# Kernel tuning notes

Measured on AMD Instinct MI355X. Metric: run time of the kernel, lower is better.

The kernel has to match this reference:

```python
import jax, jax.numpy as jnp
import numpy as np

N_NODES = 100000
N_EDGES = 625000
EMB_DIM = 128
ALPHA = 0.8  # alpha in original; effective scale is alpha/2 = 0.4


def setup_inputs() -> dict:
    key = jax.random.key(0)
    k1, k2, k3, k4, k5 = jax.random.split(key, 5)
    x = jax.random.normal(k1, (N_NODES, EMB_DIM), dtype=jnp.float32)
    e = jax.random.normal(k2, (N_NODES, EMB_DIM), dtype=jnp.float32)
    hg_vals = jax.random.uniform(k3, (N_EDGES,), dtype=jnp.float32)
    hg_rows = jax.random.randint(k4, (N_EDGES,), 0, N_NODES, dtype=jnp.int32)
    hg_cols = jax.random.randint(k5, (N_EDGES,), 0, N_NODES, dtype=jnp.int32)
    t = jnp.zeros((), dtype=jnp.float32)
    return {"t": t, "x": x, "e": e, "hg_vals": hg_vals,
            "hg_rows": hg_rows, "hg_cols": hg_cols}


def reference(t, x, e, hg_vals, hg_rows, hg_cols):
    # f = spmm((alpha/2) * HG, x) - x + e, with alpha = 0.8 (constant per entry)
    n = x.shape[0]
    scale = ALPHA / 2.0
    # gather source node features per nonzero, scale by edge value
    msgs = (scale * hg_vals)[:, None] * x[hg_cols]          # [nnz, d]
    prop = jax.ops.segment_sum(msgs, hg_rows, num_segments=n)  # [N, d]
    return prop - x + e
```

## Files before the change

### kernel.cpp

```cpp
#include <hip/hip_runtime.h>
#include <hip/hip_fp16.h>


#define EMB_DIM 128
#define Q_SLOTS 32
#define CAP 16
#define OVF_MAX 8192

struct __align__(8) half4_t { __half2 a, b; };
typedef float f32x4 __attribute__((ext_vector_type(4)));

__global__ void prep_kernel(const int* __restrict__ rows,
                            const int* __restrict__ cols,
                            const float* __restrict__ vals,
                            int* __restrict__ counts,
                            int2* __restrict__ slots,
                            int* __restrict__ ovf_cursor,
                            int4* __restrict__ ovf,
                            int n_edges,
                            const f32x4* __restrict__ x4,
                            half4_t* __restrict__ xh4,
                            int n_x4) {
    int i = blockIdx.x * blockDim.x + threadIdx.x;
    if (i < n_x4) {
        f32x4 f = __builtin_nontemporal_load(x4 + i);
        half4_t h;
        h.a = __floats2half2_rn(f.x, f.y);
        h.b = __floats2half2_rn(f.z, f.w);
        xh4[i] = h;
    }
    if (i < n_edges) {
        int   r  = __builtin_nontemporal_load(rows + i);
        int   c  = __builtin_nontemporal_load(cols + i);
        float vv = __builtin_nontemporal_load(vals + i);
        int2 p;
        p.x = c;
        p.y = __float_as_int(0.4f * vv);
        int pos = atomicAdd(&counts[r], 1);
        if (pos < CAP) {
            slots[(size_t)r * CAP + pos] = p;
        } else {
            int o = atomicAdd(ovf_cursor, 1);
            if (o < OVF_MAX) ovf[o] = make_int4(r, p.x, p.y, 0);
        }
    }
}

__global__ void gather_fp16_kernel(const half4_t* __restrict__ xh4,
                                   const f32x4* __restrict__ e4,
                                   const int* __restrict__ counts,
                                   const int2* __restrict__ slots,
                                   const int* __restrict__ ovf_cursor,
                                   const int4* __restrict__ ovf,
                                   f32x4* __restrict__ out4, int n_nodes) {
    int tid = blockIdx.x * blockDim.x + threadIdx.x;
    int row = tid >> 5;
    int q   = tid & 31;
    if (row >= n_nodes) return;

    int cfull = counts[row];
    int n = (cfull < CAP) ? cfull : CAP;
    const long long* b = (const long long*)(slots + (size_t)row * CAP);

    long long pp = 0;
    if (q < n) pp = __builtin_nontemporal_load(b + q);
    int myc = (int)(pp & 0xffffffffLL);
    int myv = (int)(pp >> 32);

    float4 acc = make_float4(0.f, 0.f, 0.f, 0.f);
    int nm1 = n - 1;

    for (int base = 0; base < n; base += 8) {
        int   col[8];
        float v[8];
#pragma unroll
        for (int k = 0; k < 8; ++k) {
            int j  = base + k;
            int jc = (j < n) ? j : nm1;
            col[k] = __shfl(myc, jc, 32);
            int vi = __shfl(myv, jc, 32);
            v[k]   = (j < n) ? __int_as_float(vi) : 0.f;
        }
        half4_t hv[8];
#pragma unroll
        for (int k = 0; k < 8; ++k) {
            hv[k] = xh4[col[k] * Q_SLOTS + q];
        }
#pragma unroll
        for (int k = 0; k < 8; ++k) {
            float2 f0 = __half22float2(hv[k].a);
            float2 f1 = __half22float2(hv[k].b);
            acc.x = fmaf(v[k], f0.x, acc.x);
            acc.y = fmaf(v[k], f0.y, acc.y);
            acc.z = fmaf(v[k], f1.x, acc.z);
            acc.w = fmaf(v[k], f1.y, acc.w);
        }
    }

    if (cfull > CAP) {
        int cnt = *ovf_cursor;
        cnt = (cnt < OVF_MAX) ? cnt : OVF_MAX;
        for (int k = 0; k < cnt; ++k) {
            int4 en = ovf[k];
            if (en.x == row) {
                float vv = __int_as_float(en.z);
                half4_t hv = xh4[en.y * Q_SLOTS + q];
                float2 f0 = __half22float2(hv.a);
                float2 f1 = __half22float2(hv.b);
                acc.x = fmaf(vv, f0.x, acc.x);
                acc.y = fmaf(vv, f0.y, acc.y);
                acc.z = fmaf(vv, f1.x, acc.z);
                acc.w = fmaf(vv, f1.y, acc.w);
            }
        }
    }

    int idx = row * Q_SLOTS + q;
    half4_t hx = xh4[idx];
    float2 x0 = __half22float2(hx.a);
    float2 x1 = __half22float2(hx.b);
    f32x4 er = __builtin_nontemporal_load(e4 + idx);
    f32x4 o;
    o.x = acc.x + er.x - x0.x;
    o.y = acc.y + er.y - x0.y;
    o.z = acc.z + er.z - x1.x;
    o.w = acc.w + er.w - x1.y;
    __builtin_nontemporal_store(o, out4 + idx);
}

__global__ void gather_f32_kernel(const f32x4* __restrict__ x4,
                                  const f32x4* __restrict__ e4,
                                  const int* __restrict__ counts,
                                  const int2* __restrict__ slots,
                                  const int* __restrict__ ovf_cursor,
                                  const int4* __restrict__ ovf,
                                  f32x4* __restrict__ out4, int n_nodes) {
    int tid = blockIdx.x * blockDim.x + threadIdx.x;
    int row = tid >> 5;
    int q   = tid & 31;
    if (row >= n_nodes) return;

    int cfull = counts[row];
    int n = (cfull < CAP) ? cfull : CAP;
    const long long* b = (const long long*)(slots + (size_t)row * CAP);

    long long pp = 0;
    if (q < n) pp = __builtin_nontemporal_load(b + q);
    int myc = (int)(pp & 0xffffffffLL);
    int myv = (int)(pp >> 32);

    float4 acc = make_float4(0.f, 0.f, 0.f, 0.f);
    int nm1 = n - 1;

    for (int base = 0; base < n; base += 8) {
        int   col[8];
        float v[8];
#pragma unroll
        for (int k = 0; k < 8; ++k) {
            int j  = base + k;
            int jc = (j < n) ? j : nm1;
            col[k] = __shfl(myc, jc, 32);
            int vi = __shfl(myv, jc, 32);
            v[k]   = (j < n) ? __int_as_float(vi) : 0.f;
        }
        f32x4 xv[8];
#pragma unroll
        for (int k = 0; k < 8; ++k) {
            xv[k] = x4[col[k] * Q_SLOTS + q];
        }
#pragma unroll
        for (int k = 0; k < 8; ++k) {
            acc.x = fmaf(v[k], xv[k].x, acc.x);
            acc.y = fmaf(v[k], xv[k].y, acc.y);
            acc.z = fmaf(v[k], xv[k].z, acc.z);
            acc.w = fmaf(v[k], xv[k].w, acc.w);
        }
    }

    if (cfull > CAP) {
        int cnt = *ovf_cursor;
        cnt = (cnt < OVF_MAX) ? cnt : OVF_MAX;
        for (int k = 0; k < cnt; ++k) {
            int4 en = ovf[k];
            if (en.x == row) {
                float vv = __int_as_float(en.z);
                f32x4 m = x4[en.y * Q_SLOTS + q];
                acc.x = fmaf(vv, m.x, acc.x);
                acc.y = fmaf(vv, m.y, acc.y);
                acc.z = fmaf(vv, m.z, acc.z);
                acc.w = fmaf(vv, m.w, acc.w);
            }
        }
    }

    int idx = row * Q_SLOTS + q;
    f32x4 xr = x4[idx];
    f32x4 er = __builtin_nontemporal_load(e4 + idx);
    f32x4 o;
    o.x = acc.x + er.x - xr.x;
    o.y = acc.y + er.y - xr.y;
    o.z = acc.z + er.z - xr.z;
    o.w = acc.w + er.w - xr.w;
    __builtin_nontemporal_store(o, out4 + idx);
}

__global__ void build_chain_kernel(const int* __restrict__ rows,
                                   const int* __restrict__ cols,
                                   const float* __restrict__ vals,
                                   int* __restrict__ head,
                                   int4* __restrict__ nodes, int n_edges) {
    int i = blockIdx.x * blockDim.x + threadIdx.x;
    if (i >= n_edges) return;
    int r = rows[i];
    int prev = atomicExch(&head[r], i);
    nodes[i] = make_int4(cols[i], __float_as_int(0.4f * vals[i]), prev, 0);
}
__global__ void gather_chain_kernel(const float2* __restrict__ x2,
                                    const float2* __restrict__ e2,
                                    const int* __restrict__ head,
                                    const int4* __restrict__ nodes,
                                    float2* __restrict__ out2, int n_nodes) {
    int tid = blockIdx.x * blockDim.x + threadIdx.x;
    int row = tid >> 6, q = tid & 63;
    if (row >= n_nodes) return;
    float2 acc = make_float2(0.f, 0.f);
    int j = head[row];
    if (j >= 0) {
        int4 nd = nodes[j];
        for (;;) {
            int4 nd2;
            bool more = (nd.z >= 0);
            if (more) nd2 = nodes[nd.z];
            float v = __int_as_float(nd.y);
            float2 xv = x2[nd.x * 64 + q];
            acc.x = fmaf(v, xv.x, acc.x);
            acc.y = fmaf(v, xv.y, acc.y);
            if (!more) break;
            nd = nd2;
        }
    }
    int idx = row * 64 + q;
    float2 xr = x2[idx], er = e2[idx];
    out2[idx] = make_float2(acc.x + er.x - xr.x, acc.y + er.y - xr.y);
}

extern "C" void kernel_launch(void* const* d_in, const int* in_sizes, int n_in,
                              void* d_out, int out_size, void* d_ws, size_t ws_size,
                              hipStream_t stream) {
    const float* x    = (const float*)d_in[1];
    const float* e    = (const float*)d_in[2];
    const float* vals = (const float*)d_in[3];
    const int*   rows = (const int*)d_in[4];
    const int*   cols = (const int*)d_in[5];
    float* out = (float*)d_out;

    const int n_edges = in_sizes[3];
    const int n_nodes = in_sizes[1] / EMB_DIM;
    const int n_x4    = n_nodes * Q_SLOTS;

    size_t need_a = (size_t)OVF_MAX * sizeof(int4) +
                    (size_t)n_x4 * sizeof(half4_t) +
                    (size_t)n_nodes * CAP * sizeof(int2) +
                    (size_t)(n_nodes + 1) * sizeof(int);
    size_t need_b = (size_t)OVF_MAX * sizeof(int4) +
                    (size_t)n_nodes * CAP * sizeof(int2) +
                    (size_t)(n_nodes + 1) * sizeof(int);

    if (ws_size >= need_a) {
        int4*    ovf        = (int4*)d_ws;
        half4_t* xh4        = (half4_t*)(ovf + OVF_MAX);
        int2*    slots      = (int2*)(xh4 + (size_t)n_x4);
        int*     counts     = (int*)(slots + (size_t)n_nodes * CAP);
        int*     ovf_cursor = counts + n_nodes;

        hipMemsetAsync(counts, 0, (size_t)(n_nodes + 1) * sizeof(int), stream);

        int pt = (n_x4 > n_edges) ? n_x4 : n_edges;
        int pb = (pt + 255) / 256;
        prep_kernel<<<pb, 256, 0, stream>>>(rows, cols, vals, counts, slots,
                                            ovf_cursor, ovf, n_edges,
                                            (const f32x4*)x, xh4, n_x4);

        long long gt = (long long)n_nodes * 32;
        int gb = (int)((gt + 255) / 256);
        gather_fp16_kernel<<<gb, 256, 0, stream>>>(xh4, (const f32x4*)e,
                                                   counts, slots,
                                                   ovf_cursor, ovf,
                                                   (f32x4*)out, n_nodes);
    } else if (ws_size >= need_b) {
        int4* ovf        = (int4*)d_ws;
        int2* slots      = (int2*)(ovf + OVF_MAX);
        int*  counts     = (int*)(slots + (size_t)n_nodes * CAP);
        int*  ovf_cursor = counts + n_nodes;

        hipMemsetAsync(counts, 0, (size_t)(n_nodes + 1) * sizeof(int), stream);

        int eb = (n_edges + 255) / 256;
        prep_kernel<<<eb, 256, 0, stream>>>(rows, cols, vals, counts, slots,
                                            ovf_cursor, ovf, n_edges,
                                            (const f32x4*)x, (half4_t*)0, 0);

        long long gt = (long long)n_nodes * 32;
        int gb = (int)((gt + 255) / 256);
        gather_f32_kernel<<<gb, 256, 0, stream>>>((const f32x4*)x,
                                                  (const f32x4*)e,
                                                  counts, slots,
                                                  ovf_cursor, ovf,
                                                  (f32x4*)out, n_nodes);
    } else {
        int4* nodes = (int4*)d_ws;
        int*  head  = (int*)(nodes + n_edges);
        hipMemsetAsync(head, 0xFF, (size_t)n_nodes * sizeof(int), stream);
        int eb = (n_edges + 255) / 256;
        build_chain_kernel<<<eb, 256, 0, stream>>>(rows, cols, vals, head,
                                                   nodes, n_edges);
        long long gt = (long long)n_nodes * 64;
        int gb = (int)((gt + 255) / 256);
        gather_chain_kernel<<<gb, 256, 0, stream>>>((const float2*)x,
                                                    (const float2*)e,
                                                    head, nodes,
                                                    (float2*)out, n_nodes);
    }
}
```

Before: 209.1 us.

## Bin edges into 32-row coarse buckets and sort within block in LDS

Result: slower. 238.5 us (+14.1%).

```diff
diff --git a/kernel.cpp b/kernel.cpp
--- a/kernel.cpp
+++ b/kernel.cpp
@@ -4,17 +4,19 @@
 
 #define EMB_DIM 128
 #define Q_SLOTS 32
-#define CAP 16
+#define RPB 32
+#define CAP_C 384
 #define OVF_MAX 8192
 
 struct __align__(8) half4_t { __half2 a, b; };
 typedef float f32x4 __attribute__((ext_vector_type(4)));
+typedef unsigned long long u64;
 
 __global__ void prep_kernel(const int* __restrict__ rows,
                             const int* __restrict__ cols,
                             const float* __restrict__ vals,
-                            int* __restrict__ counts,
-                            int2* __restrict__ slots,
+                            int* __restrict__ ccnt,
+                            u64* __restrict__ coarse,
                             int* __restrict__ ovf_cursor,
                             int4* __restrict__ ovf,
                             int n_edges,
@@ -33,175 +35,141 @@
         int   r  = __builtin_nontemporal_load(rows + i);
         int   c  = __builtin_nontemporal_load(cols + i);
         float vv = __builtin_nontemporal_load(vals + i);
-        int2 p;
-        p.x = c;
-        p.y = __float_as_int(0.4f * vv);
-        int pos = atomicAdd(&counts[r], 1);
-        if (pos < CAP) {
-            slots[(size_t)r * CAP + pos] = p;
+        int b = r >> 5;
+        int pos = atomicAdd(&ccnt[b], 1);
+        unsigned lo = (unsigned)(c | ((r & (RPB - 1)) << 17));
+        unsigned hi = (unsigned)__float_as_int(0.4f * vv);
+        u64 pv = (u64)lo | ((u64)hi << 32);
+        if (pos < CAP_C) {
+            __builtin_nontemporal_store(pv, coarse + (size_t)b * CAP_C + pos);
         } else {
             int o = atomicAdd(ovf_cursor, 1);
-            if (o < OVF_MAX) ovf[o] = make_int4(r, p.x, p.y, 0);
-        }
-    }
-}
-
-__global__ void gather_fp16_kernel(const half4_t* __restrict__ xh4,
-                                   const f32x4* __restrict__ e4,
-                                   const int* __restrict__ counts,
-                                   const int2* __restrict__ slots,
-                                   const int* __restrict__ ovf_cursor,
-                                   const int4* __restrict__ ovf,
-                                   f32x4* __restrict__ out4, int n_nodes) {
-    int tid = blockIdx.x * blockDim.x + threadIdx.x;
-    int row = tid >> 5;
-    int q   = tid & 31;
-    if (row >= n_nodes) return;
-
-    int cfull = counts[row];
-    int n = (cfull < CAP) ? cfull : CAP;
-    const long long* b = (const long long*)(slots + (size_t)row * CAP);
-
-    long long pp = 0;
-    if (q < n) pp = __builtin_nontemporal_load(b + q);
-    int myc = (int)(pp & 0xffffffffLL);
-    int myv = (int)(pp >> 32);
-
-    float4 acc = make_float4(0.f, 0.f, 0.f, 0.f);
-    int nm1 = n - 1;
-
-    for (int base = 0; base < n; base += 8) {
-        int   col[8];
-        float v[8];
-#pragma unroll
-        for (int k = 0; k < 8; ++k) {
-            int j  = base + k;
-            int jc = (j < n) ? j : nm1;
-            col[k] = __shfl(myc, jc, 32);
-            int vi = __shfl(myv, jc, 32);
-            v[k]   = (j < n) ? __int_as_float(vi) : 0.f;
-        }
-        half4_t hv[8];
-#pragma unroll
-        for (int k = 0; k < 8; ++k) {
-            hv[k] = xh4[col[k] * Q_SLOTS + q];
-        }
-#pragma unroll
-        for (int k = 0; k < 8; ++k) {
-            float2 f0 = __half22float2(hv[k].a);
-            float2 f1 = __half22float2(hv[k].b);
-            acc.x = fmaf(v[k], f0.x, acc.x);
-            acc.y = fmaf(v[k], f0.y, acc.y);
-            acc.z = fmaf(v[k], f1.x, acc.z);
-            acc.w = fmaf(v[k], f1.y, acc.w);
-        }
-    }
-
-    if (cfull > CAP) {
-        int cnt = *ovf_cursor;
-        cnt = (cnt < OVF_MAX) ? cnt : OVF_MAX;
-        for (int k = 0; k < cnt; ++k) {
-            int4 en = ovf[k];
-            if (en.x == row) {
-                float vv = __int_as_float(en.z);
-                half4_t hv = xh4[en.y * Q_SLOTS + q];
-                float2 f0 = __half22float2(hv.a);
-                float2 f1 = __half22float2(hv.b);
-                acc.x = fmaf(vv, f0.x, acc.x);
-                acc.y = fmaf(vv, f0.y, acc.y);
-                acc.z = fmaf(vv, f1.x, acc.z);
-                acc.w = fmaf(vv, f1.y, acc.w);
-            }
-        }
-    }
-
-    int idx = row * Q_SLOTS + q;
-    half4_t hx = xh4[idx];
-    float2 x0 = __half22float2(hx.a);
-    float2 x1 = __half22float2(hx.b);
-    f32x4 er = __builtin_nontemporal_load(e4 + idx);
-    f32x4 o;
-    o.x = acc.x + er.x - x0.x;
-    o.y = acc.y + er.y - x0.y;
-    o.z = acc.z + er.z - x1.x;
-    o.w = acc.w + er.w - x1.y;
-    __builtin_nontemporal_store(o, out4 + idx);
-}
-
-__global__ void gather_f32_kernel(const f32x4* __restrict__ x4,
-                                  const f32x4* __restrict__ e4,
-                                  const int* __restrict__ counts,
-                                  const int2* __restrict__ slots,
-                                  const int* __restrict__ ovf_cursor,
-                                  const int4* __restrict__ ovf,
-                                  f32x4* __restrict__ out4, int n_nodes) {
-    int tid = blockIdx.x * blockDim.x + threadIdx.x;
-    int row = tid >> 5;
-    int q   = tid & 31;
-    if (row >= n_nodes) return;
-
-    int cfull = counts[row];
-    int n = (cfull < CAP) ? cfull : CAP;
-    const long long* b = (const long long*)(slots + (size_t)row * CAP);
-
-    long long pp = 0;
-    if (q < n) pp = __builtin_nontemporal_load(b + q);
-    int myc = (int)(pp & 0xffffffffLL);
-    int myv = (int)(pp >> 32);
-
-    float4 acc = make_float4(0.f, 0.f, 0.f, 0.f);
-    int nm1 = n - 1;
-
-    for (int base = 0; base < n; base += 8) {
-        int   col[8];
-        float v[8];
-#pragma unroll
-        for (int k = 0; k < 8; ++k) {
-            int j  = base + k;
-            int jc = (j < n) ? j : nm1;
-            col[k] = __shfl(myc, jc, 32);
-            int vi = __shfl(myv, jc, 32);
-            v[k]   = (j < n) ? __int_as_float(vi) : 0.f;
-        }
-        f32x4 xv[8];
-#pragma unroll
-        for (int k = 0; k < 8; ++k) {
-            xv[k] = x4[col[k] * Q_SLOTS + q];
-        }
-#pragma unroll
-        for (int k = 0; k < 8; ++k) {
-            acc.x = fmaf(v[k], xv[k].x, acc.x);
-            acc.y = fmaf(v[k], xv[k].y, acc.y);
-            acc.z = fmaf(v[k], xv[k].z, acc.z);
-            acc.w = fmaf(v[k], xv[k].w, acc.w);
-        }
-    }
-
-    if (cfull > CAP) {
-        int cnt = *ovf_cursor;
-        cnt = (cnt < OVF_MAX) ? cnt : OVF_MAX;
-        for (int k = 0; k < cnt; ++k) {
-            int4 en = ovf[k];
-            if (en.x == row) {
-                float vv = __int_as_float(en.z);
-                f32x4 m = x4[en.y * Q_SLOTS + q];
-                acc.x = fmaf(vv, m.x, acc.x);
-                acc.y = fmaf(vv, m.y, acc.y);
-                acc.z = fmaf(vv, m.z, acc.z);
-                acc.w = fmaf(vv, m.w, acc.w);
-            }
-        }
-    }
-
-    int idx = row * Q_SLOTS + q;
-    f32x4 xr = x4[idx];
-    f32x4 er = __builtin_nontemporal_load(e4 + idx);
-    f32x4 o;
-    o.x = acc.x + er.x - xr.x;
-    o.y = acc.y + er.y - xr.y;
-    o.z = acc.z + er.z - xr.z;
-    o.w = acc.w + er.w - xr.w;
-    __builtin_nontemporal_store(o, out4 + idx);
+            if (o < OVF_MAX) ovf[o] = make_int4(r, c, __float_as_int(0.4f * vv), 0);
+        }
+    }
+}
+
+__global__ void __launch_bounds__(256, 8)
+bin_gather_kernel(const half4_t* __restrict__ xh4,
+                  const f32x4* __restrict__ e4,
+                  const int* __restrict__ ccnt,
+                  const u64* __restrict__ coarse,
+                  const int* __restrict__ ovf_cursor,
+                  const int4* __restrict__ ovf,
+                  f32x4* __restrict__ out4, int n_nodes) {
+    __shared__ int  s_cnt[RPB];
+    __shared__ int  s_off[RPB + 1];
+    __shared__ int  s_cur[RPB];
+    __shared__ int2 s_raw[CAP_C];
+    __shared__ int2 s_ent[CAP_C];
+    __shared__ int  s_ovf;
+
+    int b = blockIdx.x;
+    int t = threadIdx.x;
+    int row_base = b * RPB;
+
+    int nb = ccnt[b];
+    nb = (nb < CAP_C) ? nb : CAP_C;
+
+    if (t < RPB) s_cnt[t] = 0;
+    if (t == 0) s_ovf = *ovf_cursor;
+    __syncthreads();
+
+    const u64* cb = coarse + (size_t)b * CAP_C;
+    for (int j = t; j < nb; j += 256) {
+        u64 pv = __builtin_nontemporal_load(cb + j);
+        int lo = (int)(pv & 0xffffffffULL);
+        int hi = (int)(pv >> 32);
+        s_raw[j] = make_int2(lo, hi);
+        atomicAdd(&s_cnt[(lo >> 17) & (RPB - 1)], 1);
+    }
+    __syncthreads();
+    if (t < 64) {
+        int v = (t < RPB) ? s_cnt[t] : 0;
+        int incl = v;
+#pragma unroll
+        for (int d = 1; d < RPB; d <<= 1) {
+            int o = __shfl_up(incl, d, 64);
+            if ((t & 63) >= d) incl += o;
+        }
+        if (t < RPB) { s_off[t + 1] = incl; s_cur[t] = incl - v; }
+        if (t == 0) s_off[0] = 0;
+    }
+    __syncthreads();
+    for (int j = t; j < nb; j += 256) {
+        int2 en = s_raw[j];
+        int r = (en.x >> 17) & (RPB - 1);
+        int pos = atomicAdd(&s_cur[r], 1);
+        s_ent[pos] = make_int2(en.x & 0x1FFFF, en.y);
+    }
+    __syncthreads();
+
+    int team = t >> 5;
+    int q    = t & 31;
+    int ocnt = s_ovf;
+    ocnt = (ocnt < OVF_MAX) ? ocnt : OVF_MAX;
+
+    for (int rr = team; rr < RPB; rr += 8) {
+        int grow = row_base + rr;
+        if (grow >= n_nodes) continue;
+        int start = s_off[rr], end = s_off[rr + 1];
+
+        float4 acc = make_float4(0.f, 0.f, 0.f, 0.f);
+        for (int jb = start; jb < end; jb += 8) {
+            int   col[8];
+            float v[8];
+#pragma unroll
+            for (int k = 0; k < 8; ++k) {
+                int j  = jb + k;
+                int jc = (j < end) ? j : end - 1;
+                int2 en = s_ent[jc];
+                col[k] = en.x;
+                v[k]   = (j < end) ? __int_as_float(en.y) : 0.f;
+            }
+            half4_t hv[8];
+#pragma unroll
+            for (int k = 0; k < 8; ++k) {
+                hv[k] = xh4[col[k] * Q_SLOTS + q];
+            }
+#pragma unroll
+            for (int k = 0; k < 8; ++k) {
+                float2 f0 = __half22float2(hv[k].a);
+                float2 f1 = __half22float2(hv[k].b);
+                acc.x = fmaf(v[k], f0.x, acc.x);
+                acc.y = fmaf(v[k], f0.y, acc.y);
+                acc.z = fmaf(v[k], f1.x, acc.z);
+                acc.w = fmaf(v[k], f1.y, acc.w);
+            }
+        }
+
+        if (ocnt > 0) {
+            for (int k = 0; k < ocnt; ++k) {
+                int4 en = ovf[k];
+                if (en.x == grow) {
+                    float vv = __int_as_float(en.z);
+                    half4_t hv = xh4[en.y * Q_SLOTS + q];
+                    float2 f0 = __half22float2(hv.a);
+                    float2 f1 = __half22float2(hv.b);
+                    acc.x = fmaf(vv, f0.x, acc.x);
+                    acc.y = fmaf(vv, f0.y, acc.y);
+                    acc.z = fmaf(vv, f1.x, acc.z);
+                    acc.w = fmaf(vv, f1.y, acc.w);
+                }
+            }
+        }
+
+        int idx = grow * Q_SLOTS + q;
+        half4_t hx = xh4[idx];
+        float2 x0 = __half22float2(hx.a);
+        float2 x1 = __half22float2(hx.b);
+        f32x4 er = __builtin_nontemporal_load(e4 + idx);
+        f32x4 o;
+        o.x = acc.x + er.x - x0.x;
+        o.y = acc.y + er.y - x0.y;
+        o.z = acc.z + er.z - x1.x;
+        o.w = acc.w + er.w - x1.y;
+        __builtin_nontemporal_store(o, out4 + idx);
+    }
 }
 
 __global__ void build_chain_kernel(const int* __restrict__ rows,
@@ -257,56 +225,32 @@
     const int n_edges = in_sizes[3];
     const int n_nodes = in_sizes[1] / EMB_DIM;
     const int n_x4    = n_nodes * Q_SLOTS;
+    const int n_buck  = (n_nodes + RPB - 1) / RPB;
 
     size_t need_a = (size_t)OVF_MAX * sizeof(int4) +
                     (size_t)n_x4 * sizeof(half4_t) +
-                    (size_t)n_nodes * CAP * sizeof(int2) +
-                    (size_t)(n_nodes + 1) * sizeof(int);
-    size_t need_b = (size_t)OVF_MAX * sizeof(int4) +
-                    (size_t)n_nodes * CAP * sizeof(int2) +
-                    (size_t)(n_nodes + 1) * sizeof(int);
-
-    if (ws_size >= need_a) {
+                    (size_t)n_buck * CAP_C * sizeof(u64) +
+                    (size_t)(n_buck + 1) * sizeof(int);
+
+    if (ws_size >= need_a && n_nodes <= (1 << 17)) {
         int4*    ovf        = (int4*)d_ws;
         half4_t* xh4        = (half4_t*)(ovf + OVF_MAX);
-        int2*    slots      = (int2*)(xh4 + (size_t)n_x4);
-        int*     counts     = (int*)(slots + (size_t)n_nodes * CAP);
-        int*     ovf_cursor = counts + n_nodes;
-
-        hipMemsetAsync(counts, 0, (size_t)(n_nodes + 1) * sizeof(int), stream);
+        u64*     coarse     = (u64*)(xh4 + (size_t)n_x4);
+        int*     ccnt       = (int*)(coarse + (size_t)n_buck * CAP_C);
+        int*     ovf_cursor = ccnt + n_buck;
+
+        hipMemsetAsync(ccnt, 0, (size_t)(n_buck + 1) * sizeof(int), stream);
 
         int pt = (n_x4 > n_edges) ? n_x4 : n_edges;
         int pb = (pt + 255) / 256;
-        prep_kernel<<<pb, 256, 0, stream>>>(rows, cols, vals, counts, slots,
+        prep_kernel<<<pb, 256, 0, stream>>>(rows, cols, vals, ccnt, coarse,
                                             ovf_cursor, ovf, n_edges,
                                             (const f32x4*)x, xh4, n_x4);
 
-        long long gt = (long long)n_nodes * 32;
-        int gb = (int)((gt + 255) / 256);
-        gather_fp16_kernel<<<gb, 256, 0, stream>>>(xh4, (const f32x4*)e,
-                                                   counts, slots,
-                                                   ovf_cursor, ovf,
-                                                   (f32x4*)out, n_nodes);
-    } else if (ws_size >= need_b) {
-        int4* ovf        = (int4*)d_ws;
-        int2* slots      = (int2*)(ovf + OVF_MAX);
-        int*  counts     = (int*)(slots + (size_t)n_nodes * CAP);
-        int*  ovf_cursor = counts + n_nodes;
-
-        hipMemsetAsync(counts, 0, (size_t)(n_nodes + 1) * sizeof(int), stream);
-
-        int eb = (n_edges + 255) / 256;
-        prep_kernel<<<eb, 256, 0, stream>>>(rows, cols, vals, counts, slots,
-                                            ovf_cursor, ovf, n_edges,
-                                            (const f32x4*)x, (half4_t*)0, 0);
-
-        long long gt = (long long)n_nodes * 32;
-        int gb = (int)((gt + 255) / 256);
-        gather_f32_kernel<<<gb, 256, 0, stream>>>((const f32x4*)x,
-                                                  (const f32x4*)e,
-                                                  counts, slots,
-                                                  ovf_cursor, ovf,
-                                                  (f32x4*)out, n_nodes);
+        bin_gather_kernel<<<n_buck, 256, 0, stream>>>(xh4, (const f32x4*)e,
+                                                      ccnt, coarse,
+                                                      ovf_cursor, ovf,
+                                                      (f32x4*)out, n_nodes);
     } else {
         int4* nodes = (int4*)d_ws;
         int*  head  = (int*)(nodes + n_edges);
```

## Fuse prep and gather into persistent kernel with software grid barrier

Applied to the files above, without the earlier changes.

Result: slower. 366.3 us (+75.1%).

```diff
diff --git a/kernel.cpp b/kernel.cpp
--- a/kernel.cpp
+++ b/kernel.cpp
@@ -9,62 +9,53 @@
 
 struct __align__(8) half4_t { __half2 a, b; };
 typedef float f32x4 __attribute__((ext_vector_type(4)));
-
-__global__ void prep_kernel(const int* __restrict__ rows,
-                            const int* __restrict__ cols,
-                            const float* __restrict__ vals,
-                            int* __restrict__ counts,
-                            int2* __restrict__ slots,
-                            int* __restrict__ ovf_cursor,
-                            int4* __restrict__ ovf,
-                            int n_edges,
-                            const f32x4* __restrict__ x4,
-                            half4_t* __restrict__ xh4,
-                            int n_x4) {
-    int i = blockIdx.x * blockDim.x + threadIdx.x;
+typedef unsigned long long u64;
+
+
+__device__ __forceinline__ void prep_item(int i,
+    const int* __restrict__ rows, const int* __restrict__ cols,
+    const float* __restrict__ vals, int* __restrict__ counts,
+    u64* __restrict__ slots, int* __restrict__ ovf_cursor,
+    int4* __restrict__ ovf, int n_edges,
+    const f32x4* __restrict__ x4, half4_t* __restrict__ xh4, int n_x4)
+{
     if (i < n_x4) {
-        f32x4 f = __builtin_nontemporal_load(x4 + i);
+        f32x4 f = x4[i];
         half4_t h;
         h.a = __floats2half2_rn(f.x, f.y);
         h.b = __floats2half2_rn(f.z, f.w);
         xh4[i] = h;
     }
     if (i < n_edges) {
-        int   r  = __builtin_nontemporal_load(rows + i);
-        int   c  = __builtin_nontemporal_load(cols + i);
-        float vv = __builtin_nontemporal_load(vals + i);
-        int2 p;
-        p.x = c;
-        p.y = __float_as_int(0.4f * vv);
+        int   r  = rows[i];
+        int   c  = cols[i];
+        float vv = vals[i];
+        u64 pv = (u64)(unsigned)c |
+                 ((u64)(unsigned)__float_as_int(0.4f * vv) << 32);
         int pos = atomicAdd(&counts[r], 1);
         if (pos < CAP) {
-            slots[(size_t)r * CAP + pos] = p;
+            slots[(size_t)r * CAP + pos] = pv;
         } else {
             int o = atomicAdd(ovf_cursor, 1);
-            if (o < OVF_MAX) ovf[o] = make_int4(r, p.x, p.y, 0);
-        }
-    }
-}
-
-__global__ void gather_fp16_kernel(const half4_t* __restrict__ xh4,
-                                   const f32x4* __restrict__ e4,
-                                   const int* __restrict__ counts,
-                                   const int2* __restrict__ slots,
-                                   const int* __restrict__ ovf_cursor,
-                                   const int4* __restrict__ ovf,
-                                   f32x4* __restrict__ out4, int n_nodes) {
-    int tid = blockIdx.x * blockDim.x + threadIdx.x;
-    int row = tid >> 5;
-    int q   = tid & 31;
-    if (row >= n_nodes) return;
-
+            if (o < OVF_MAX)
+                ovf[o] = make_int4(r, c, __float_as_int(0.4f * vv), 0);
+        }
+    }
+}
+
+__device__ __forceinline__ void gather_row(int row, int q,
+    const half4_t* __restrict__ xh4, const f32x4* __restrict__ e4,
+    const int* __restrict__ counts, const u64* __restrict__ slots,
+    const int* __restrict__ ovf_cursor, const int4* __restrict__ ovf,
+    f32x4* __restrict__ out4)
+{
     int cfull = counts[row];
     int n = (cfull < CAP) ? cfull : CAP;
-    const long long* b = (const long long*)(slots + (size_t)row * CAP);
-
-    long long pp = 0;
+    const u64* b = slots + (size_t)row * CAP;
+
+    u64 pp = 0;
     if (q < n) pp = __builtin_nontemporal_load(b + q);
-    int myc = (int)(pp & 0xffffffffLL);
+    int myc = (int)(pp & 0xffffffffULL);
     int myv = (int)(pp >> 32);
 
     float4 acc = make_float4(0.f, 0.f, 0.f, 0.f);
@@ -128,80 +119,76 @@
     __builtin_nontemporal_store(o, out4 + idx);
 }
 
-__global__ void gather_f32_kernel(const f32x4* __restrict__ x4,
-                                  const f32x4* __restrict__ e4,
-                                  const int* __restrict__ counts,
-                                  const int2* __restrict__ slots,
-                                  const int* __restrict__ ovf_cursor,
-                                  const int4* __restrict__ ovf,
-                                  f32x4* __restrict__ out4, int n_nodes) {
+__device__ __forceinline__ void grid_barrier(int* cnt, int* flag, int nblocks)
+{
+    __syncthreads();
+    if (threadIdx.x == 0) {
+        __threadfence();
+        int v = __hip_atomic_fetch_add(cnt, 1, __ATOMIC_ACQ_REL,
+                                       __HIP_MEMORY_SCOPE_AGENT);
+        if (v == nblocks - 1) {
+            __hip_atomic_store(flag, 1, __ATOMIC_RELEASE,
+                               __HIP_MEMORY_SCOPE_AGENT);
+        } else {
+            while (!__hip_atomic_load(flag, __ATOMIC_ACQUIRE,
+                                      __HIP_MEMORY_SCOPE_AGENT)) {
+                __builtin_amdgcn_s_sleep(1);
+            }
+        }
+        __threadfence();
+    }
+    __syncthreads();
+}
+
+__global__ void __launch_bounds__(256, 8)
+fused_kernel(const int* __restrict__ rows, const int* __restrict__ cols,
+             const float* __restrict__ vals, int* counts, u64* slots,
+             int* ovf_cursor, int4* ovf, int n_edges,
+             const f32x4* __restrict__ x4, half4_t* __restrict__ xh4,
+             int n_x4, const f32x4* __restrict__ e4,
+             f32x4* __restrict__ out4, int n_nodes, int* bar)
+{
+    const int T   = gridDim.x * blockDim.x;
+    const int tid = blockIdx.x * blockDim.x + threadIdx.x;
+
+    int pt = (n_x4 > n_edges) ? n_x4 : n_edges;
+    for (int i = tid; i < pt; i += T)
+        prep_item(i, rows, cols, vals, counts, slots, ovf_cursor, ovf,
+                  n_edges, x4, xh4, n_x4);
+
+    grid_barrier(bar + 0, bar + 1, gridDim.x);
+
+    const int q = tid & 31;
+    const int rstep = T >> 5;
+    for (int row = tid >> 5; row < n_nodes; row += rstep)
+        gather_row(row, q, xh4, e4, counts, slots, ovf_cursor, ovf, out4);
+}
+
+__global__ void prep_kernel(const int* __restrict__ rows,
+                            const int* __restrict__ cols,
+                            const float* __restrict__ vals,
+                            int* counts, u64* slots, int* ovf_cursor,
+                            int4* ovf, int n_edges,
+                            const f32x4* __restrict__ x4,
+                            half4_t* __restrict__ xh4, int n_x4)
+{
+    int i = blockIdx.x * blockDim.x + threadIdx.x;
+    prep_item(i, rows, cols, vals, counts, slots, ovf_cursor, ovf,
+              n_edges, x4, xh4, n_x4);
+}
+
+__global__ void gather_kernel(const half4_t* __restrict__ xh4,
+                              const f32x4* __restrict__ e4,
+                              const int* __restrict__ counts,
+                              const u64* __restrict__ slots,
+                              const int* __restrict__ ovf_cursor,
+                              const int4* __restrict__ ovf,
+                              f32x4* __restrict__ out4, int n_nodes)
+{
     int tid = blockIdx.x * blockDim.x + threadIdx.x;
     int row = tid >> 5;
-    int q   = tid & 31;
     if (row >= n_nodes) return;
-
-    int cfull = counts[row];
-    int n = (cfull < CAP) ? cfull : CAP;
-    const long long* b = (const long long*)(slots + (size_t)row * CAP);
-
-    long long pp = 0;
-    if (q < n) pp = __builtin_nontemporal_load(b + q);
-    int myc = (int)(pp & 0xffffffffLL);
-    int myv = (int)(pp >> 32);
-
-    float4 acc = make_float4(0.f, 0.f, 0.f, 0.f);
-    int nm1 = n - 1;
-
-    for (int base = 0; base < n; base += 8) {
-        int   col[8];
-        float v[8];
-#pragma unroll
-        for (int k = 0; k < 8; ++k) {
-            int j  = base + k;
-            int jc = (j < n) ? j : nm1;
-            col[k] = __shfl(myc, jc, 32);
-            int vi = __shfl(myv, jc, 32);
-            v[k]   = (j < n) ? __int_as_float(vi) : 0.f;
-        }
-        f32x4 xv[8];
-#pragma unroll
-        for (int k = 0; k < 8; ++k) {
-            xv[k] = x4[col[k] * Q_SLOTS + q];
-        }
-#pragma unroll
-        for (int k = 0; k < 8; ++k) {
-            acc.x = fmaf(v[k], xv[k].x, acc.x);
-            acc.y = fmaf(v[k], xv[k].y, acc.y);
-            acc.z = fmaf(v[k], xv[k].z, acc.z);
-            acc.w = fmaf(v[k], xv[k].w, acc.w);
-        }
-    }
-
-    if (cfull > CAP) {
-        int cnt = *ovf_cursor;
-        cnt = (cnt < OVF_MAX) ? cnt : OVF_MAX;
-        for (int k = 0; k < cnt; ++k) {
-            int4 en = ovf[k];
-            if (en.x == row) {
-                float vv = __int_as_float(en.z);
-                f32x4 m = x4[en.y * Q_SLOTS + q];
-                acc.x = fmaf(vv, m.x, acc.x);
-                acc.y = fmaf(vv, m.y, acc.y);
-                acc.z = fmaf(vv, m.z, acc.z);
-                acc.w = fmaf(vv, m.w, acc.w);
-            }
-        }
-    }
-
-    int idx = row * Q_SLOTS + q;
-    f32x4 xr = x4[idx];
-    f32x4 er = __builtin_nontemporal_load(e4 + idx);
-    f32x4 o;
-    o.x = acc.x + er.x - xr.x;
-    o.y = acc.y + er.y - xr.y;
-    o.z = acc.z + er.z - xr.z;
-    o.w = acc.w + er.w - xr.w;
-    __builtin_nontemporal_store(o, out4 + idx);
+    gather_row(row, tid & 31, xh4, e4, counts, slots, ovf_cursor, ovf, out4);
 }
 
 __global__ void build_chain_kernel(const int* __restrict__ rows,
@@ -260,53 +247,55 @@
 
     size_t need_a = (size_t)OVF_MAX * sizeof(int4) +
                     (size_t)n_x4 * sizeof(half4_t) +
-                    (size_t)n_nodes * CAP * sizeof(int2) +
-                    (size_t)(n_nodes + 1) * sizeof(int);
-    size_t need_b = (size_t)OVF_MAX * sizeof(int4) +
-                    (size_t)n_nodes * CAP * sizeof(int2) +
-                    (size_t)(n_nodes + 1) * sizeof(int);
+                    (size_t)n_nodes * CAP * sizeof(u64) +
+                    (size_t)(n_nodes + 8) * sizeof(int);
 
     if (ws_size >= need_a) {
         int4*    ovf        = (int4*)d_ws;
         half4_t* xh4        = (half4_t*)(ovf + OVF_MAX);
-        int2*    slots      = (int2*)(xh4 + (size_t)n_x4);
+        u64*     slots      = (u64*)(xh4 + (size_t)n_x4);
         int*     counts     = (int*)(slots + (size_t)n_nodes * CAP);
         int*     ovf_cursor = counts + n_nodes;
-
-        hipMemsetAsync(counts, 0, (size_t)(n_nodes + 1) * sizeof(int), stream);
-
-        int pt = (n_x4 > n_edges) ? n_x4 : n_edges;
-        int pb = (pt + 255) / 256;
-        prep_kernel<<<pb, 256, 0, stream>>>(rows, cols, vals, counts, slots,
-                                            ovf_cursor, ovf, n_edges,
-                                            (const f32x4*)x, xh4, n_x4);
-
-        long long gt = (long long)n_nodes * 32;
-        int gb = (int)((gt + 255) / 256);
-        gather_fp16_kernel<<<gb, 256, 0, stream>>>(xh4, (const f32x4*)e,
-                                                   counts, slots,
-                                                   ovf_cursor, ovf,
-                                                   (f32x4*)out, n_nodes);
-    } else if (ws_size >= need_b) {
-        int4* ovf        = (int4*)d_ws;
-        int2* slots      = (int2*)(ovf + OVF_MAX);
-        int*  counts     = (int*)(slots + (size_t)n_nodes * CAP);
-        int*  ovf_cursor = counts + n_nodes;
-
-        hipMemsetAsync(counts, 0, (size_t)(n_nodes + 1) * sizeof(int), stream);
-
-        int eb = (n_edges + 255) / 256;
-        prep_kernel<<<eb, 256, 0, stream>>>(rows, cols, vals, counts, slots,
-                                            ovf_cursor, ovf, n_edges,
-                                            (const f32x4*)x, (half4_t*)0, 0);
-
-        long long gt = (long long)n_nodes * 32;
-        int gb = (int)((gt + 255) / 256);
-        gather_f32_kernel<<<gb, 256, 0, stream>>>((const f32x4*)x,
-                                                  (const f32x4*)e,
+        int*     bar        = counts + n_nodes + 1;
+
+        hipMemsetAsync(counts, 0, (size_t)(n_nodes + 8) * sizeof(int), stream);
+
+        static int g_blocks = -2;
+        if (g_blocks == -2) {
+            g_blocks = -1;
+            int dev = 0;
+            if (hipGetDevice(&dev) == hipSuccess) {
+                hipDeviceProp_t prop;
+                int maxb = 0;
+                if (hipGetDeviceProperties(&prop, dev) == hipSuccess &&
+                    hipOccupancyMaxActiveBlocksPerMultiprocessor(
+                        &maxb, fused_kernel, 256, 0) == hipSuccess &&
+                    maxb >= 1) {
+                    int bpc = (maxb < 8) ? maxb : 8;
+                    g_blocks = prop.multiProcessorCount * bpc;
+                }
+            }
+        }
+
+        if (g_blocks > 0) {
+            fused_kernel<<<g_blocks, 256, 0, stream>>>(
+                rows, cols, vals, counts, slots, ovf_cursor, ovf, n_edges,
+                (const f32x4*)x, xh4, n_x4, (const f32x4*)e,
+                (f32x4*)out, n_nodes, bar);
+        } else {
+            int pt = (n_x4 > n_edges) ? n_x4 : n_edges;
+            int pb = (pt + 255) / 256;
+            prep_kernel<<<pb, 256, 0, stream>>>(rows, cols, vals, counts,
+                                                slots, ovf_cursor, ovf,
+                                                n_edges, (const f32x4*)x,
+                                                xh4, n_x4);
+            long long gt = (long long)n_nodes * 32;
+            int gb = (int)((gt + 255) / 256);
+            gather_kernel<<<gb, 256, 0, stream>>>(xh4, (const f32x4*)e,
                                                   counts, slots,
                                                   ovf_cursor, ovf,
                                                   (f32x4*)out, n_nodes);
+        }
     } else {
         int4* nodes = (int4*)d_ws;
         int*  head  = (int*)(nodes + n_edges);
```
